# Kernel tuning notes

Measured on AMD Instinct MI355X. Metric: run time of the kernel, lower is better.

## Reference

```python
import jax, jax.numpy as jnp
import numpy as np

N = 50000        # num nodes
E = 800000       # num edges (avg degree 16)
NFEAT = 128
NHID = 128
NCLASS = 64


def setup_inputs() -> dict:
    key = jax.random.key(0)
    k0, k1, k2, k3 = jax.random.split(key, 4)
    x = jax.random.normal(k0, (N, NFEAT), dtype=jnp.float32)
    edge_index = jax.random.randint(k1, (2, E), 0, N)
    edge_weight = jnp.ones((E,), dtype=jnp.float32)
    # GCNConv linear weights (glorot-ish uniform), biases zero
    s1 = 1.0 / np.sqrt(NFEAT)
    W1 = jax.random.uniform(k2, (NFEAT, NHID), jnp.float32, -s1, s1)
    b1 = jnp.zeros((NHID,), jnp.float32)
    s2 = 1.0 / np.sqrt(NHID)
    W2 = jax.random.uniform(k3, (NHID, NCLASS), jnp.float32, -s2, s2)
    b2 = jnp.zeros((NCLASS,), jnp.float32)
    return {"x": x, "edge_index": edge_index, "edge_weight": edge_weight,
            "W1": W1, "b1": b1, "W2": W2, "b2": b2}


def reference(x, edge_index, edge_weight, W1, b1, W2, b2):
    n = x.shape[0]
    # add self loops (fill_value = 1.0), as GCNConv(add_self_loops=True)
    loops = jnp.arange(n)
    ei = jnp.concatenate([edge_index, jnp.stack([loops, loops])], axis=1)
    ew = jnp.concatenate([edge_weight, jnp.ones((n,), x.dtype)])
    row, col = ei[0], ei[1]
    # symmetric gcn normalization: D^-1/2 A D^-1/2
    deg = jax.ops.segment_sum(ew, col, num_segments=n)
    dinv = jnp.where(deg > 0, jax.lax.rsqrt(deg), 0.0)
    norm = dinv[row] * ew * dinv[col]        # [E+N]

    def conv(h, W, b):
        h = h @ W                                   # [N, F_out]
        msg = norm[:, None] * h[row]                # gather + scale, [E+N, F_out]
        return jax.ops.segment_sum(msg, col, num_segments=n) + b

    h = jax.nn.relu(conv(x, W1, b1))  # dropout p=0.0 -> identity
    out = conv(h, W2, b2)
    # F.normalize(p=2, dim=-1)
    nrm = jnp.linalg.norm(out, axis=-1, keepdims=True)
    return out / jnp.maximum(nrm, 1e-12)
```

## Files before the change

kernel.cpp:

```cpp
#include <hip/hip_runtime.h>

#define NF 128
#define NC 64
#define SLICES 64

typedef short bf16x8 __attribute__((ext_vector_type(8)));
typedef float f32x4 __attribute__((ext_vector_type(4)));

__device__ __forceinline__ unsigned f2bf(float f) {
    unsigned u = __float_as_uint(f);
    return (u + 0x7FFFu + ((u >> 16) & 1u)) >> 16;
}
__device__ __forceinline__ float bf2f(unsigned h) { return __uint_as_float(h << 16); }

__global__ __launch_bounds__(256) void prep_fused(const int* __restrict__ col,
                                                  unsigned short* __restrict__ eoff16,
                                                  unsigned short* __restrict__ C16,
                                                  const float* __restrict__ W1,
                                                  const float* __restrict__ W2,
                                                  unsigned short* __restrict__ Wt1,
                                                  unsigned short* __restrict__ Wt2,
                                                  const float* __restrict__ X,
                                                  unsigned* __restrict__ Xb2,
                                                  int N, int E, int SL, int nh,
                                                  int CRB, int WTB, int XCB) {
    __shared__ unsigned hist[12544];
    const int b = blockIdx.x;
    const int tid = threadIdx.x;
    if (b < CRB) {
        const int j = b >> 1;
        const int h = b & 1;
        const int nlo = h * nh;
        const int nhi = min(N, nlo + nh);
        const int words = (nhi - nlo + 1) >> 1;
        for (int i = tid; i < words; i += 256) hist[i] = 0;
        __syncthreads();
        const int e0 = j * SL, e1 = min(E, e0 + SL);
        for (int e = e0 + tid; e < e1; e += 256) {
            int c = col[e];
            if (c >= nlo && c < nhi) {
                int cl = c - nlo;
                unsigned sh = (cl & 1) * 16;
                unsigned old = atomicAdd(&hist[cl >> 1], 1u << sh);
                eoff16[e] = (unsigned short)((old >> sh) & 0xffffu);
            }
        }
        __syncthreads();
        unsigned* Cw = (unsigned*)(C16 + (size_t)j * N + nlo);
        for (int i = tid; i < words; i += 256) Cw[i] = hist[i];
    } else if (b < CRB + WTB) {
        int i = (b - CRB) * 256 + tid;
        if (i < 128 * 128) {
            int k = i >> 7, n = i & 127;
            Wt1[n * 128 + k] = (unsigned short)f2bf(W1[i]);
        } else {
            int j = i - 128 * 128;
            if (j < 128 * 64) {
                int k = j >> 6, n = j & 63;
                Wt2[n * 128 + k] = (unsigned short)f2bf(W2[j]);
            }
        }
    } else {
        const float4* X4 = (const float4*)X;
        uint2* O = (uint2*)Xb2;
        int items = N * 32;
        for (int i = (b - CRB - WTB) * 256 + tid; i < items; i += XCB * 256) {
            float4 v = X4[i];
            O[i] = make_uint2(f2bf(v.x) | (f2bf(v.y) << 16),
                              f2bf(v.z) | (f2bf(v.w) << 16));
        }
    }
}

__global__ __launch_bounds__(256) void scanC_kernel(unsigned short* __restrict__ C16,
                                                    int* __restrict__ tot, int N) {
    int n = blockIdx.x * 256 + threadIdx.x;
    if (n >= N) return;
    int t = 0;
#pragma unroll 4
    for (int j = 0; j < SLICES; ++j) {
        size_t idx = (size_t)j * N + n;
        int v = C16[idx];
        C16[idx] = (unsigned short)t;
        t += v;
    }
    tot[n] = t;
}

__global__ __launch_bounds__(256) void scan_blocks(const int* __restrict__ cnt,
                                                   int* __restrict__ excl,
                                                   int* __restrict__ bsum, int N) {
    __shared__ int sh[256];
    int t = threadIdx.x;
    int base = blockIdx.x * 1024 + t * 4;
    int v0 = base + 0 < N ? cnt[base + 0] : 0;
    int v1 = base + 1 < N ? cnt[base + 1] : 0;
    int v2 = base + 2 < N ? cnt[base + 2] : 0;
    int v3 = base + 3 < N ? cnt[base + 3] : 0;
    int s = v0 + v1 + v2 + v3;
    sh[t] = s;
    __syncthreads();
    for (int off = 1; off < 256; off <<= 1) {
        int x = (t >= off) ? sh[t - off] : 0;
        __syncthreads();
        sh[t] += x;
        __syncthreads();
    }
    int incl = sh[t];
    int exclT = incl - s;
    if (t == 255) bsum[blockIdx.x] = incl;
    if (base + 0 < N) excl[base + 0] = exclT;
    if (base + 1 < N) excl[base + 1] = exclT + v0;
    if (base + 2 < N) excl[base + 2] = exclT + v0 + v1;
    if (base + 3 < N) excl[base + 3] = exclT + v0 + v1 + v2;
}

__global__ void scan_sums(int* __restrict__ bsum, int nb) {
    int run = 0;
    for (int i = 0; i < nb; ++i) { int v = bsum[i]; bsum[i] = run; run += v; }
    bsum[nb] = run;
}

__global__ __launch_bounds__(256) void scan_add(int* __restrict__ excl,
                                                const int* __restrict__ bsum,
                                                int N, int nb) {
    int i = blockIdx.x * 256 + threadIdx.x;
    if (i < N) excl[i] += bsum[i >> 10];
    if (i == 0) excl[N] = bsum[nb];
}

__global__ __launch_bounds__(256) void scatter_gemm1_fused(const int* __restrict__ row,
                                                           const int* __restrict__ col,
                                                           const float* __restrict__ ew,
                                                           const int* __restrict__ rowPtr,
                                                           const unsigned short* __restrict__ Coff16,
                                                           const unsigned short* __restrict__ eoff16,
                                                           unsigned* __restrict__ csru,
                                                           const unsigned short* __restrict__ Xb,
                                                           const unsigned short* __restrict__ Wt1,
                                                           unsigned short* __restrict__ H1c,
                                                           int N, int E, int SL, int SB) {
    __shared__ char XsB[16384];
    __shared__ char WsB[32768];
    const int tid = threadIdx.x;
    if ((int)blockIdx.x < SB) {
        const int j = blockIdx.x >> 3;
        const int sub = blockIdx.x & 7;
        const int e0 = j * SL, e1 = min(E, e0 + SL);
        const int per = ((e1 - e0) + 7) >> 3;
        const int lo = min(e1, e0 + sub * per);
        const int hi = min(e1, lo + per);
        const unsigned short* Crow = Coff16 + (size_t)j * N;
        for (int e = lo + tid; e < hi; e += 256) {
            int c = col[e];
            int idx = rowPtr[c] + (int)Crow[c] + (int)eoff16[e];
            csru[idx] = ((unsigned)row[e] << 16) | f2bf(ew[e]);
        }
        return;
    }
    const int bm0 = ((int)blockIdx.x - SB) * 64;
    {
        int r = tid >> 2, q4 = (tid & 3) * 4;
        const uint4* src = (const uint4*)(Xb + (size_t)min(bm0 + r, N - 1) * 128);
#pragma unroll
        for (int qq = 0; qq < 4; ++qq) {
            int kb = (q4 + qq) * 16;
            *(uint4*)(XsB + r * 256 + (kb ^ ((r & 7) << 4))) = src[q4 + qq];
        }
    }
    {
        const uint4* src = (const uint4*)Wt1;
#pragma unroll
        for (int t = 0; t < 8; ++t) {
            int i = t * 256 + tid;
            int n = i >> 4, kb = (i & 15) * 16;
            *(uint4*)(WsB + n * 256 + (kb ^ ((n & 7) << 4))) = src[i];
        }
    }
    __syncthreads();
    const int w = tid >> 6, l = tid & 63;
    const int lr = l & 15, lg = l >> 4;
    f32x4 acc[8] = {};
#pragma unroll
    for (int kk = 0; kk < 4; ++kk) {
        int r = w * 16 + lr;
        bf16x8 a = *(const bf16x8*)(XsB + r * 256 + ((kk * 64 + lg * 16) ^ ((r & 7) << 4)));
        bf16x8 b[8];
#pragma unroll
        for (int nt = 0; nt < 8; ++nt) {
            int n = nt * 16 + lr;
            b[nt] = *(const bf16x8*)(WsB + n * 256 + ((kk * 64 + lg * 16) ^ ((n & 7) << 4)));
        }
#pragma unroll
        for (int nt = 0; nt < 8; ++nt)
            acc[nt] = __builtin_amdgcn_mfma_f32_16x16x32_bf16(a, b[nt], acc[nt], 0, 0, 0);
    }
#pragma unroll
    for (int reg = 0; reg < 4; ++reg) {
        int node = bm0 + w * 16 + lg * 4 + reg;
        if (node < N) {
#pragma unroll
            for (int nt = 0; nt < 8; ++nt)
                H1c[((size_t)(nt >> 1) * N + node) * 32 + (nt & 1) * 16 + lr] =
                    (unsigned short)f2bf(acc[nt][reg]);
        }
    }
}

__global__ __launch_bounds__(256) void gemm2_mfma(const unsigned short* __restrict__ A,
                                                  const unsigned short* __restrict__ Wt2,
                                                  unsigned short* __restrict__ H, int N) {
    __shared__ char XsB[32768];
    __shared__ char WsB[16384];
    const int tid = threadIdx.x;
    const int bm0 = blockIdx.x * 128;
    {
        int k16 = tid & 15, r0 = tid >> 4;
        for (int it = 0; it < 8; ++it) {
            int r = it * 16 + r0;
            int node = min(bm0 + r, N - 1);
            uint4 g = *(const uint4*)(A + (size_t)node * 128 + k16 * 8);
            *(uint4*)(XsB + r * 256 + ((k16 * 16) ^ ((r & 7) << 4))) = g;
        }
    }
    {
        const uint4* src = (const uint4*)Wt2;
        for (int t = 0; t < 4; ++t) {
            int i = t * 256 + tid;
            int n = i >> 4, kb = (i & 15) * 16;
            *(uint4*)(WsB + n * 256 + (kb ^ ((n & 7) << 4))) = src[i];
        }
    }
    __syncthreads();
    const int w = tid >> 6, l = tid & 63;
    const int lr = l & 15, lg = l >> 4;
    f32x4 acc[2][4] = {};
#pragma unroll
    for (int kk = 0; kk < 4; ++kk) {
        bf16x8 a[2], b[4];
#pragma unroll
        for (int mt = 0; mt < 2; ++mt) {
            int r = w * 32 + mt * 16 + lr;
            a[mt] = *(const bf16x8*)(XsB + r * 256 + ((kk * 64 + lg * 16) ^ ((r & 7) << 4)));
        }
#pragma unroll
        for (int nt = 0; nt < 4; ++nt) {
            int n = nt * 16 + lr;
            b[nt] = *(const bf16x8*)(WsB + n * 256 + ((kk * 64 + lg * 16) ^ ((n & 7) << 4)));
        }
#pragma unroll
        for (int mt = 0; mt < 2; ++mt)
#pragma unroll
            for (int nt = 0; nt < 4; ++nt)
                acc[mt][nt] = __builtin_amdgcn_mfma_f32_16x16x32_bf16(a[mt], b[nt], acc[mt][nt], 0, 0, 0);
    }
#pragma unroll
    for (int mt = 0; mt < 2; ++mt)
#pragma unroll
        for (int reg = 0; reg < 4; ++reg) {
            int node = bm0 + w * 32 + mt * 16 + lg * 4 + reg;
            if (node < N) {
#pragma unroll
                for (int nt = 0; nt < 4; ++nt)
                    H[(size_t)node * 64 + nt * 16 + lr] = (unsigned short)f2bf(acc[mt][nt][reg]);
            }
        }
}

__global__ __launch_bounds__(256) void deg_dinv_kernel(const int* __restrict__ rowPtr,
                                                       const unsigned* __restrict__ csru,
                                                       float* __restrict__ dinv, int N) {
    int idx = blockIdx.x * 256 + threadIdx.x;
    int n = idx >> 4, l = idx & 15;
    if (n >= N) return;
    int beg = rowPtr[n], end = rowPtr[n + 1];
    float s = 0.f;
    for (int i = beg + l; i < end; i += 16) s += bf2f(csru[i] & 0xffffu);
#pragma unroll
    for (int off = 8; off; off >>= 1) s += __shfl_xor(s, off, 16);
    if (l == 0) dinv[n] = rsqrtf(s + 1.0f);
}

__global__ __launch_bounds__(256) void norm_w_kernel(unsigned* __restrict__ csru,
                                                     const float* __restrict__ dinv, int E) {
    int i = blockIdx.x * 256 + threadIdx.x;
    if (i >= E) return;
    unsigned p = csru[i];
    float w = bf2f(p & 0xffffu) * dinv[p >> 16];
    csru[i] = (p & 0xffff0000u) | f2bf(w);
}

__global__ __launch_bounds__(256) void agg_gather1(const int* __restrict__ rowPtr,
                                                   const unsigned* __restrict__ csru,
                                                   const unsigned* __restrict__ H1c,
                                                   const float* __restrict__ dinv,
                                                   const float2* __restrict__ b2,
                                                   unsigned* __restrict__ out1, int N) {
    int n = blockIdx.x * 16 + (threadIdx.x >> 4);
    int l = threadIdx.x & 15;
    if (n >= N) return;
    float dn = dinv[n];
    float s = dn * dn;
    int beg = rowPtr[n], end = rowPtr[n + 1];
#pragma unroll
    for (int c = 0; c < 4; ++c) {
        const unsigned* P = H1c + (size_t)c * N * 16;
        float accx = 0.f, accy = 0.f;
        int j = beg;
        for (; j + 4 <= end; j += 4) {
            unsigned p0 = csru[j + 0], p1 = csru[j + 1], p2 = csru[j + 2], p3 = csru[j + 3];
            float w0 = bf2f(p0 & 0xffffu), w1 = bf2f(p1 & 0xffffu);
            float w2 = bf2f(p2 & 0xffffu), w3 = bf2f(p3 & 0xffffu);
            unsigned v0 = P[(size_t)(p0 >> 16) * 16 + l];
            unsigned v1 = P[(size_t)(p1 >> 16) * 16 + l];
            unsigned v2 = P[(size_t)(p2 >> 16) * 16 + l];
            unsigned v3 = P[(size_t)(p3 >> 16) * 16 + l];
            accx += w0 * bf2f(v0 & 0xffffu); accy += w0 * bf2f(v0 >> 16);
            accx += w1 * bf2f(v1 & 0xffffu); accy += w1 * bf2f(v1 >> 16);
            accx += w2 * bf2f(v2 & 0xffffu); accy += w2 * bf2f(v2 >> 16);
            accx += w3 * bf2f(v3 & 0xffffu); accy += w3 * bf2f(v3 >> 16);
        }
        for (; j < end; ++j) {
            unsigned p = csru[j];
            float w = bf2f(p & 0xffffu);
            unsigned v = P[(size_t)(p >> 16) * 16 + l];
            accx += w * bf2f(v & 0xffffu); accy += w * bf2f(v >> 16);
        }
        unsigned hv = P[(size_t)n * 16 + l];
        float2 bb = b2[c * 16 + l];
        float ox = fmaxf(fmaf(dn, accx, s * bf2f(hv & 0xffffu)) + bb.x, 0.f);
        float oy = fmaxf(fmaf(dn, accy, s * bf2f(hv >> 16)) + bb.y, 0.f);
        out1[(size_t)n * 64 + c * 16 + l] = f2bf(ox) | (f2bf(oy) << 16);
    }
}

__global__ __launch_bounds__(256) void agg_gather2(const int* __restrict__ rowPtr,
                                                   const unsigned* __restrict__ csru,
                                                   const unsigned* __restrict__ H3u,
                                                   const float* __restrict__ dinv,
                                                   const float2* __restrict__ b2,
                                                   float2* __restrict__ out2, int N) {
    int n = (blockIdx.x * 256 + threadIdx.x) >> 5;
    int l = threadIdx.x & 31;
    if (n >= N) return;
    float dn = dinv[n];
    float accx = 0.f, accy = 0.f;
    int beg = rowPtr[n], end = rowPtr[n + 1];
    int j = beg;
    for (; j + 4 <= end; j += 4) {
        unsigned p0 = csru[j + 0], p1 = csru[j + 1], p2 = csru[j + 2], p3 = csru[j + 3];
        float w0 = bf2f(p0 & 0xffffu), w1 = bf2f(p1 & 0xffffu);
        float w2 = bf2f(p2 & 0xffffu), w3 = bf2f(p3 & 0xffffu);
        unsigned v0 = H3u[(size_t)(p0 >> 16) * 32 + l];
        unsigned v1 = H3u[(size_t)(p1 >> 16) * 32 + l];
        unsigned v2 = H3u[(size_t)(p2 >> 16) * 32 + l];
        unsigned v3 = H3u[(size_t)(p3 >> 16) * 32 + l];
        accx += w0 * bf2f(v0 & 0xffffu); accy += w0 * bf2f(v0 >> 16);
        accx += w1 * bf2f(v1 & 0xffffu); accy += w1 * bf2f(v1 >> 16);
        accx += w2 * bf2f(v2 & 0xffffu); accy += w2 * bf2f(v2 >> 16);
        accx += w3 * bf2f(v3 & 0xffffu); accy += w3 * bf2f(v3 >> 16);
    }
    for (; j < end; ++j) {
        unsigned p = csru[j];
        float w = bf2f(p & 0xffffu);
        unsigned v = H3u[(size_t)(p >> 16) * 32 + l];
        accx += w * bf2f(v & 0xffffu); accy += w * bf2f(v >> 16);
    }
    unsigned hv = H3u[(size_t)n * 32 + l];
    float2 bb = b2[l];
    float s = dn * dn;
    float vx = fmaf(dn, accx, s * bf2f(hv & 0xffffu)) + bb.x;
    float vy = fmaf(dn, accy, s * bf2f(hv >> 16)) + bb.y;
    float ss = vx * vx + vy * vy;
#pragma unroll
    for (int off = 16; off; off >>= 1) ss += __shfl_xor(ss, off, 64);
    float scale = 1.0f / fmaxf(sqrtf(ss), 1e-12f);
    out2[(size_t)n * 32 + l] = make_float2(vx * scale, vy * scale);
}

extern "C" void kernel_launch(void* const* d_in, const int* in_sizes, int n_in,
                              void* d_out, int out_size, void* d_ws, size_t ws_size,
                              hipStream_t stream) {
    const float* x  = (const float*)d_in[0];
    const int*   ei = (const int*)d_in[1];
    const float* ew = (const float*)d_in[2];
    const float* W1 = (const float*)d_in[3];
    const float* b1 = (const float*)d_in[4];
    const float* W2 = (const float*)d_in[5];
    const float* b2 = (const float*)d_in[6];
    float* out = (float*)d_out;
    const int N = in_sizes[0] / NF;
    const int E = in_sizes[2];
    const int* row = ei;
    const int* col = ei + E;
    const int NB = (N + 1023) / 1024;
    const int SL = (E + SLICES - 1) / SLICES;
    const int nh = (N + 1) / 2;

    char* ws = (char*)d_ws;
    size_t off = 0;
    auto take = [&](size_t bytes) {
        char* p = ws + off;
        off = (off + bytes + 255) & ~(size_t)255;
        return p;
    };
    float* dinv   = (float*)take((size_t)N * 4);
    int*   tot    = (int*)  take((size_t)N * 4);
    int*   rowPtr = (int*)  take((size_t)(N + 1) * 4);
    unsigned short* eoff16 = (unsigned short*)take((size_t)E * 2);
    int*   bsum   = (int*)  take((size_t)(NB + 1) * 4);
    unsigned short* C16    = (unsigned short*)take((size_t)SLICES * N * 2);
    unsigned* csru = (unsigned*)take((size_t)E * 4);
    unsigned short* Xb   = (unsigned short*)take((size_t)N * NF * 2);
    unsigned short* H1c  = (unsigned short*)take((size_t)N * NF * 2);
    unsigned short* relu = (unsigned short*)take((size_t)N * NF * 2);
    unsigned short* Wt1  = (unsigned short*)take(128 * 128 * 2);
    unsigned short* Wt2  = (unsigned short*)take(64 * 128 * 2);
    unsigned short* H3 = H1c;

    const int CRB = 2 * SLICES, WTB = 96, XCB = 1024;
    prep_fused<<<CRB + WTB + XCB, 256, 0, stream>>>(col, eoff16, C16, W1, W2, Wt1, Wt2,
                                                    x, (unsigned*)Xb, N, E, SL, nh,
                                                    CRB, WTB, XCB);

    scanC_kernel<<<(N + 255) / 256, 256, 0, stream>>>(C16, tot, N);
    scan_blocks<<<NB, 256, 0, stream>>>(tot, rowPtr, bsum, N);
    scan_sums<<<1, 1, 0, stream>>>(bsum, NB);
    scan_add<<<(N + 255) / 256, 256, 0, stream>>>(rowPtr, bsum, N, NB);

    const int SB = 8 * SLICES;
    const int GB = (N + 63) / 64;
    scatter_gemm1_fused<<<SB + GB, 256, 0, stream>>>(row, col, ew, rowPtr, C16, eoff16,
                                                     csru, Xb, Wt1, H1c, N, E, SL, SB);

    deg_dinv_kernel<<<(N * 16 + 255) / 256, 256, 0, stream>>>(rowPtr, csru, dinv, N);
    norm_w_kernel<<<(E + 255) / 256, 256, 0, stream>>>(csru, dinv, E);

    agg_gather1<<<(N * 16 + 255) / 256, 256, 0, stream>>>(rowPtr, csru, (const unsigned*)H1c,
                                                          dinv, (const float2*)b1,
                                                          (unsigned*)relu, N);

    gemm2_mfma<<<(N + 127) / 128, 256, 0, stream>>>(relu, Wt2, H3, N);
    agg_gather2<<<(N * 32 + 255) / 256, 256, 0, stream>>>(rowPtr, csru, (const unsigned*)H3,
                                                          dinv, (const float2*)b2,
                                                          (float2*)out, N);
}
```

Baseline: 165.7 us.

## Fuse slice scan with block scan and split layer-1 aggregation per plane

Merges the per-node slice prefix kernel with the block scan, so the totals array and one launch go away and the block size becomes 256 nodes. The layer-1 gather is split into four launches, one per 32-column plane of H1, so each launch touches only a 3.2MB plane that can stay in L2 instead of streaming all four planes in a single pass. This costs extra launches and rereads rowPtr and csru four times. Loads in agg_gather2 are also reordered so the gathers are issued before the weight decodes.

```diff
diff --git a/kernel.cpp b/kernel.cpp
--- a/kernel.cpp
+++ b/kernel.cpp
@@ -72,33 +72,23 @@
     }
 }
 
-__global__ __launch_bounds__(256) void scanC_kernel(unsigned short* __restrict__ C16,
-                                                    int* __restrict__ tot, int N) {
-    int n = blockIdx.x * 256 + threadIdx.x;
-    if (n >= N) return;
-    int t = 0;
-#pragma unroll 4
-    for (int j = 0; j < SLICES; ++j) {
-        size_t idx = (size_t)j * N + n;
-        int v = C16[idx];
-        C16[idx] = (unsigned short)t;
-        t += v;
-    }
-    tot[n] = t;
-}
-
-__global__ __launch_bounds__(256) void scan_blocks(const int* __restrict__ cnt,
-                                                   int* __restrict__ excl,
-                                                   int* __restrict__ bsum, int N) {
+__global__ __launch_bounds__(256) void scanCB(unsigned short* __restrict__ C16,
+                                              int* __restrict__ excl,
+                                              int* __restrict__ bsum, int N) {
     __shared__ int sh[256];
     int t = threadIdx.x;
-    int base = blockIdx.x * 1024 + t * 4;
-    int v0 = base + 0 < N ? cnt[base + 0] : 0;
-    int v1 = base + 1 < N ? cnt[base + 1] : 0;
-    int v2 = base + 2 < N ? cnt[base + 2] : 0;
-    int v3 = base + 3 < N ? cnt[base + 3] : 0;
-    int s = v0 + v1 + v2 + v3;
-    sh[t] = s;
+    int n = blockIdx.x * 256 + t;
+    int run = 0;
+    if (n < N) {
+#pragma unroll 4
+        for (int j = 0; j < SLICES; ++j) {
+            size_t idx = (size_t)j * N + n;
+            int v = C16[idx];
+            C16[idx] = (unsigned short)run;
+            run += v;
+        }
+    }
+    sh[t] = run;
     __syncthreads();
     for (int off = 1; off < 256; off <<= 1) {
         int x = (t >= off) ? sh[t - off] : 0;
@@ -107,12 +97,8 @@
         __syncthreads();
     }
     int incl = sh[t];
-    int exclT = incl - s;
     if (t == 255) bsum[blockIdx.x] = incl;
-    if (base + 0 < N) excl[base + 0] = exclT;
-    if (base + 1 < N) excl[base + 1] = exclT + v0;
-    if (base + 2 < N) excl[base + 2] = exclT + v0 + v1;
-    if (base + 3 < N) excl[base + 3] = exclT + v0 + v1 + v2;
+    if (n < N) excl[n] = incl - run;
 }
 
 __global__ void scan_sums(int* __restrict__ bsum, int nb) {
@@ -125,7 +111,7 @@
                                                 const int* __restrict__ bsum,
                                                 int N, int nb) {
     int i = blockIdx.x * 256 + threadIdx.x;
-    if (i < N) excl[i] += bsum[i >> 10];
+    if (i < N) excl[i] += bsum[i >> 8];
     if (i == 0) excl[N] = bsum[nb];
 }
 
@@ -290,48 +276,45 @@
     csru[i] = (p & 0xffff0000u) | f2bf(w);
 }
 
-__global__ __launch_bounds__(256) void agg_gather1(const int* __restrict__ rowPtr,
-                                                   const unsigned* __restrict__ csru,
-                                                   const unsigned* __restrict__ H1c,
-                                                   const float* __restrict__ dinv,
-                                                   const float2* __restrict__ b2,
-                                                   unsigned* __restrict__ out1, int N) {
-    int n = blockIdx.x * 16 + (threadIdx.x >> 4);
+__global__ __launch_bounds__(256) void agg1_plane(const int* __restrict__ rowPtr,
+                                                  const unsigned* __restrict__ csru,
+                                                  const unsigned* __restrict__ P,
+                                                  const float* __restrict__ dinv,
+                                                  const float2* __restrict__ b2,
+                                                  unsigned* __restrict__ out1,
+                                                  int N, int c) {
+    int n = (blockIdx.x * 256 + threadIdx.x) >> 4;
     int l = threadIdx.x & 15;
     if (n >= N) return;
     float dn = dinv[n];
+    float accx = 0.f, accy = 0.f;
+    int beg = rowPtr[n], end = rowPtr[n + 1];
+    int j = beg;
+    for (; j + 4 <= end; j += 4) {
+        unsigned p0 = csru[j + 0], p1 = csru[j + 1], p2 = csru[j + 2], p3 = csru[j + 3];
+        unsigned v0 = P[(size_t)(p0 >> 16) * 16 + l];
+        unsigned v1 = P[(size_t)(p1 >> 16) * 16 + l];
+        unsigned v2 = P[(size_t)(p2 >> 16) * 16 + l];
+        unsigned v3 = P[(size_t)(p3 >> 16) * 16 + l];
+        float w0 = bf2f(p0 & 0xffffu), w1 = bf2f(p1 & 0xffffu);
+        float w2 = bf2f(p2 & 0xffffu), w3 = bf2f(p3 & 0xffffu);
+        accx += w0 * bf2f(v0 & 0xffffu); accy += w0 * bf2f(v0 >> 16);
+        accx += w1 * bf2f(v1 & 0xffffu); accy += w1 * bf2f(v1 >> 16);
+        accx += w2 * bf2f(v2 & 0xffffu); accy += w2 * bf2f(v2 >> 16);
+        accx += w3 * bf2f(v3 & 0xffffu); accy += w3 * bf2f(v3 >> 16);
+    }
+    for (; j < end; ++j) {
+        unsigned p = csru[j];
+        float w = bf2f(p & 0xffffu);
+        unsigned v = P[(size_t)(p >> 16) * 16 + l];
+        accx += w * bf2f(v & 0xffffu); accy += w * bf2f(v >> 16);
+    }
+    unsigned hv = P[(size_t)n * 16 + l];
+    float2 bb = b2[c * 16 + l];
     float s = dn * dn;
-    int beg = rowPtr[n], end = rowPtr[n + 1];
-#pragma unroll
-    for (int c = 0; c < 4; ++c) {
-        const unsigned* P = H1c + (size_t)c * N * 16;
-        float accx = 0.f, accy = 0.f;
-        int j = beg;
-        for (; j + 4 <= end; j += 4) {
-            unsigned p0 = csru[j + 0], p1 = csru[j + 1], p2 = csru[j + 2], p3 = csru[j + 3];
-            float w0 = bf2f(p0 & 0xffffu), w1 = bf2f(p1 & 0xffffu);
-            float w2 = bf2f(p2 & 0xffffu), w3 = bf2f(p3 & 0xffffu);
-            unsigned v0 = P[(size_t)(p0 >> 16) * 16 + l];
-            unsigned v1 = P[(size_t)(p1 >> 16) * 16 + l];
-            unsigned v2 = P[(size_t)(p2 >> 16) * 16 + l];
-            unsigned v3 = P[(size_t)(p3 >> 16) * 16 + l];
-            accx += w0 * bf2f(v0 & 0xffffu); accy += w0 * bf2f(v0 >> 16);
-            accx += w1 * bf2f(v1 & 0xffffu); accy += w1 * bf2f(v1 >> 16);
-            accx += w2 * bf2f(v2 & 0xffffu); accy += w2 * bf2f(v2 >> 16);
-            accx += w3 * bf2f(v3 & 0xffffu); accy += w3 * bf2f(v3 >> 16);
-        }
-        for (; j < end; ++j) {
-            unsigned p = csru[j];
-            float w = bf2f(p & 0xffffu);
-            unsigned v = P[(size_t)(p >> 16) * 16 + l];
-            accx += w * bf2f(v & 0xffffu); accy += w * bf2f(v >> 16);
-        }
-        unsigned hv = P[(size_t)n * 16 + l];
-        float2 bb = b2[c * 16 + l];
-        float ox = fmaxf(fmaf(dn, accx, s * bf2f(hv & 0xffffu)) + bb.x, 0.f);
-        float oy = fmaxf(fmaf(dn, accy, s * bf2f(hv >> 16)) + bb.y, 0.f);
-        out1[(size_t)n * 64 + c * 16 + l] = f2bf(ox) | (f2bf(oy) << 16);
-    }
+    float ox = fmaxf(fmaf(dn, accx, s * bf2f(hv & 0xffffu)) + bb.x, 0.f);
+    float oy = fmaxf(fmaf(dn, accy, s * bf2f(hv >> 16)) + bb.y, 0.f);
+    out1[(size_t)n * 64 + c * 16 + l] = f2bf(ox) | (f2bf(oy) << 16);
 }
 
 __global__ __launch_bounds__(256) void agg_gather2(const int* __restrict__ rowPtr,
@@ -349,12 +332,12 @@
     int j = beg;
     for (; j + 4 <= end; j += 4) {
         unsigned p0 = csru[j + 0], p1 = csru[j + 1], p2 = csru[j + 2], p3 = csru[j + 3];
-        float w0 = bf2f(p0 & 0xffffu), w1 = bf2f(p1 & 0xffffu);
-        float w2 = bf2f(p2 & 0xffffu), w3 = bf2f(p3 & 0xffffu);
         unsigned v0 = H3u[(size_t)(p0 >> 16) * 32 + l];
         unsigned v1 = H3u[(size_t)(p1 >> 16) * 32 + l];
         unsigned v2 = H3u[(size_t)(p2 >> 16) * 32 + l];
         unsigned v3 = H3u[(size_t)(p3 >> 16) * 32 + l];
+        float w0 = bf2f(p0 & 0xffffu), w1 = bf2f(p1 & 0xffffu);
+        float w2 = bf2f(p2 & 0xffffu), w3 = bf2f(p3 & 0xffffu);
         accx += w0 * bf2f(v0 & 0xffffu); accy += w0 * bf2f(v0 >> 16);
         accx += w1 * bf2f(v1 & 0xffffu); accy += w1 * bf2f(v1 >> 16);
         accx += w2 * bf2f(v2 & 0xffffu); accy += w2 * bf2f(v2 >> 16);
@@ -393,7 +376,7 @@
     const int E = in_sizes[2];
     const int* row = ei;
     const int* col = ei + E;
-    const int NB = (N + 1023) / 1024;
+    const int NB2 = (N + 255) / 256;
     const int SL = (E + SLICES - 1) / SLICES;
     const int nh = (N + 1) / 2;
 
@@ -405,10 +388,9 @@
         return p;
     };
     float* dinv   = (float*)take((size_t)N * 4);
-    int*   tot    = (int*)  take((size_t)N * 4);
     int*   rowPtr = (int*)  take((size_t)(N + 1) * 4);
     unsigned short* eoff16 = (unsigned short*)take((size_t)E * 2);
-    int*   bsum   = (int*)  take((size_t)(NB + 1) * 4);
+    int*   bsum   = (int*)  take((size_t)(NB2 + 1) * 4);
     unsigned short* C16    = (unsigned short*)take((size_t)SLICES * N * 2);
     unsigned* csru = (unsigned*)take((size_t)E * 4);
     unsigned short* Xb   = (unsigned short*)take((size_t)N * NF * 2);
@@ -423,10 +405,9 @@
                                                     x, (unsigned*)Xb, N, E, SL, nh,
                                                     CRB, WTB, XCB);
 
-    scanC_kernel<<<(N + 255) / 256, 256, 0, stream>>>(C16, tot, N);
-    scan_blocks<<<NB, 256, 0, stream>>>(tot, rowPtr, bsum, N);
-    scan_sums<<<1, 1, 0, stream>>>(bsum, NB);
-    scan_add<<<(N + 255) / 256, 256, 0, stream>>>(rowPtr, bsum, N, NB);
+    scanCB<<<NB2, 256, 0, stream>>>(C16, rowPtr, bsum, N);
+    scan_sums<<<1, 1, 0, stream>>>(bsum, NB2);
+    scan_add<<<(N + 255) / 256, 256, 0, stream>>>(rowPtr, bsum, N, NB2);
 
     const int SB = 8 * SLICES;
     const int GB = (N + 63) / 64;
@@ -436,9 +417,11 @@
     deg_dinv_kernel<<<(N * 16 + 255) / 256, 256, 0, stream>>>(rowPtr, csru, dinv, N);
     norm_w_kernel<<<(E + 255) / 256, 256, 0, stream>>>(csru, dinv, E);
 
-    agg_gather1<<<(N * 16 + 255) / 256, 256, 0, stream>>>(rowPtr, csru, (const unsigned*)H1c,
-                                                          dinv, (const float2*)b1,
-                                                          (unsigned*)relu, N);
+    for (int c = 0; c < 4; ++c) {
+        agg1_plane<<<(N * 16 + 255) / 256, 256, 0, stream>>>(
+            rowPtr, csru, (const unsigned*)(H1c + (size_t)c * N * 32), dinv,
+            (const float2*)b1, (unsigned*)relu, N, c);
+    }
 
     gemm2_mfma<<<(N + 127) / 128, 256, 0, stream>>>(relu, Wt2, H3, N);
     agg_gather2<<<(N * 32 + 255) / 256, 256, 0, stream>>>(rowPtr, csru, (const unsigned*)H3,
```

New measurement: 181.8 us. +9.7%, slower.
